# Optimization experiments

Measured on AMD Instinct MI355X. Metric: run time of the kernel, lower is better.

## Reference

```python
import jax, jax.numpy as jnp
import numpy as np

B, H0, W0, C = 8, 112, 112, 192
NH, WS, SS = 6, 7, 3
HID = 4 * C


def _rel_pos_index(ws):
    coords = np.stack(np.meshgrid(np.arange(ws), np.arange(ws), indexing='ij'))  # [2,ws,ws]
    flat = coords.reshape(2, -1)
    rel = flat[:, :, None] - flat[:, None, :]          # [2,N,N]
    rel = rel.transpose(1, 2, 0).copy()                # [N,N,2]
    rel[:, :, 0] += ws - 1
    rel[:, :, 1] += ws - 1
    rel[:, :, 0] *= 2 * ws - 1
    return rel.sum(-1)                                 # [N,N]


def _attn_mask(Hp, Wp, ws, ss):
    # 0 / -100 mask for shifted windows, identical to torch get_attn_mask
    img = np.zeros((Hp, Wp))
    cnt = 0
    for hs in (slice(0, -ws), slice(-ws, -ss), slice(-ss, None)):
        for wsl in (slice(0, -ws), slice(-ws, -ss), slice(-ss, None)):
            img[hs, wsl] = cnt
            cnt += 1
    mw = img.reshape(Hp // ws, ws, Wp // ws, ws).transpose(0, 2, 1, 3).reshape(-1, ws * ws)
    am = mw[:, None, :] - mw[:, :, None]
    return np.where(am != 0, np.float32(-100.0), np.float32(0.0)).astype(np.float32)  # [nW,N,N]


def _ln(x, g, b, eps=1e-5):
    mu = jnp.mean(x, axis=-1, keepdims=True)
    var = jnp.mean(jnp.square(x - mu), axis=-1, keepdims=True)
    return (x - mu) * jax.lax.rsqrt(var + eps) * g + b


def setup_inputs() -> dict:
    key = jax.random.key(0)
    ks = jax.random.split(key, 8)
    p = lambda k, s: jax.random.normal(k, s, jnp.float32) * 0.02
    return {
        'query': jax.random.normal(ks[0], (B, H0 * W0, C), jnp.float32),
        'norm1_g': jnp.ones((C,), jnp.float32), 'norm1_b': jnp.zeros((C,), jnp.float32),
        'qkv_w': p(ks[1], (C, 3 * C)), 'qkv_b': jnp.zeros((3 * C,), jnp.float32),
        'rpb_table': p(ks[2], ((2 * WS - 1) ** 2, NH)),
        'proj_w': p(ks[3], (C, C)), 'proj_b': jnp.zeros((C,), jnp.float32),
        'norm2_g': jnp.ones((C,), jnp.float32), 'norm2_b': jnp.zeros((C,), jnp.float32),
        'fc1_w': p(ks[4], (C, HID)), 'fc1_b': jnp.zeros((HID,), jnp.float32),
        'fc2_w': p(ks[5], (HID, C)), 'fc2_b': jnp.zeros((C,), jnp.float32),
        'H': H0, 'W': W0,
    }


def reference(query, norm1_g, norm1_b, qkv_w, qkv_b, rpb_table, proj_w, proj_b,
              norm2_g, norm2_b, fc1_w, fc1_b, fc2_w, fc2_b, H, W):
    Bq, L, Cq = query.shape
    ws, ss, nh = WS, SS, NH
    hd = Cq // nh
    N = ws * ws
    # ---- W-MSA branch ----
    x = _ln(query, norm1_g, norm1_b).reshape(Bq, H, W, Cq)
    # H, W chosen divisible by ws -> pad branch is a no-op
    x = jnp.roll(x, (-ss, -ss), axis=(1, 2))            # cyclic shift
    nWh, nWw = H // ws, W // ws
    # window partition -> [B*nW, N, C]
    xw = x.reshape(Bq, nWh, ws, nWw, ws, Cq).transpose(0, 1, 3, 2, 4, 5).reshape(-1, N, Cq)
    qkv = (xw @ qkv_w + qkv_b).reshape(-1, N, 3, nh, hd).transpose(2, 0, 3, 1, 4)
    q, k, v = qkv[0] * (hd ** -0.5), qkv[1], qkv[2]     # [B_,nh,N,hd]
    attn = jnp.einsum('bhnd,bhmd->bhnm', q, k)
    bias = rpb_table[_rel_pos_index(ws).reshape(-1)].reshape(N, N, nh).transpose(2, 0, 1)
    attn = attn + bias[None]
    mask = jnp.asarray(_attn_mask(H, W, ws, ss))        # [nW,N,N]
    nW = mask.shape[0]
    attn = attn.reshape(Bq, nW, nh, N, N) + mask[None, :, None]
    attn = jax.nn.softmax(attn.reshape(-1, nh, N, N), axis=-1)
    out = jnp.einsum('bhnm,bhmd->bhnd', attn, v).transpose(0, 2, 1, 3).reshape(-1, N, Cq)
    out = out @ proj_w + proj_b
    # window reverse + reverse shift
    x = out.reshape(Bq, nWh, nWw, ws, ws, Cq).transpose(0, 1, 3, 2, 4, 5).reshape(Bq, H, W, Cq)
    x = jnp.roll(x, (ss, ss), axis=(1, 2)).reshape(Bq, H * W, Cq)
    x = query + x
    # ---- MLP branch ----
    h = _ln(x, norm2_g, norm2_b)
    h = jax.nn.gelu(h @ fc1_w + fc1_b, approximate=False)
    return x + (h @ fc2_w + fc2_b)
```

## Files before the change

### kernel.cpp

```cpp
#include <hip/hip_runtime.h>
#include <hip/hip_bf16.h>
#include <math.h>

using bf16 = __hip_bfloat16;
typedef __bf16 bf16x8 __attribute__((ext_vector_type(8)));
typedef __bf16 bf16x4 __attribute__((ext_vector_type(4)));
typedef float floatx4 __attribute__((ext_vector_type(4)));

__device__ __forceinline__ float bf2f(bf16 x) { return __bfloat162float(x); }
__device__ __forceinline__ bf16 f2bf(float x) { return __float2bfloat16(x); }

__device__ __forceinline__ float loadExt(const void* p, long i, int f32) {
  return f32 ? ((const float*)p)[i] : bf2f(((const bf16*)p)[i]);
}
__device__ __forceinline__ void storeExt(void* p, long i, int f32, float v) {
  if (f32) ((float*)p)[i] = v;
  else     ((bf16*)p)[i] = f2bf(v);
}

#define GLOAD16(gp, lp)                                                       \
  __builtin_amdgcn_global_load_lds(                                           \
      (const __attribute__((address_space(1))) void*)(gp),                    \
      (__attribute__((address_space(3))) void*)(lp), 16, 0, 0)

__global__ void detect_kernel(const unsigned int* __restrict__ q, int* __restrict__ flag) {
  const int lane = threadIdx.x;
  const unsigned int w = q[lane];
  const unsigned int lo = w & 0xffffu;
  const unsigned int e = (lo >> 7) & 0xffu;
  const bool ok = (lo == 0u) || (e >= 100u && e <= 141u);
  const unsigned long long m = __ballot(ok);
  if (lane == 0) flag[0] = (__popcll(m) == 64) ? 1 : 0;
}

__global__ void cvt_params_kernel(const int* __restrict__ flagp,
                                  const void* qkv_b, const void* proj_b,
                                  const void* n1g, const void* n1b,
                                  const void* n2g, const void* n2b,
                                  const void* fc1_b, const void* fc2_b,
                                  const void* rpb, bf16* __restrict__ dst) {
  const int f32 = (flagp[0] == 0);
  int i = blockIdx.x * blockDim.x + threadIdx.x;
  if (i >= 3510) return;
  const void* src; int j = i;
  if      (j < 576)  { src = qkv_b; }
  else if ((j -= 576)  < 192) { src = proj_b; }
  else if ((j -= 192)  < 192) { src = n1g; }
  else if ((j -= 192)  < 192) { src = n1b; }
  else if ((j -= 192)  < 192) { src = n2g; }
  else if ((j -= 192)  < 192) { src = n2b; }
  else if ((j -= 192)  < 768) { src = fc1_b; }
  else if ((j -= 768)  < 192) { src = fc2_b; }
  else { j -= 192; src = rpb; }
  dst[i] = f2bf(loadExt(src, j, f32));
}

__global__ void cvtT_kernel(const int* __restrict__ flagp, const void* __restrict__ src,
                            bf16* __restrict__ dst, int K, int N) {
  const int f32 = (flagp[0] == 0);
  int i = blockIdx.x * blockDim.x + threadIdx.x;
  if (i >= K * N) return;
  int n = i / K, k = i - n * K;
  dst[i] = f2bf(loadExt(src, (long)k * N + n, f32));
}

__global__ void biastab_kernel(const bf16* __restrict__ rpb,
                               bf16* __restrict__ btab) {
  int i = blockIdx.x * blockDim.x + threadIdx.x;
  if (i >= 6 * 2450) return;
  int head = i / 2450, r = i - head * 2450;
  int n = r / 50, m = r - n * 50;
  float v = 0.f;
  if (n < 49 && m < 49) {
    int r1 = n / 7, c1 = n - 7 * r1, r2 = m / 7, c2 = m - 7 * r2;
    v = bf2f(rpb[((r1 - r2 + 6) * 13 + (c1 - c2 + 6)) * 6 + head]);
  }
  btab[i] = f2bf(v);
}

__global__ __launch_bounds__(256) void ln_kernel(const int* __restrict__ flagp, int ext,
                                                 const void* __restrict__ x,
                                                 const bf16* __restrict__ g,
                                                 const bf16* __restrict__ b,
                                                 bf16* __restrict__ out) {
  const int f32 = ext && (flagp[0] == 0);
  const long row = (long)blockIdx.x * 4 + (threadIdx.x >> 6);
  const int lane = threadIdx.x & 63;
  const long gbase = row * 192;
  float v0 = loadExt(x, gbase + lane, f32);
  float v1 = loadExt(x, gbase + lane + 64, f32);
  float v2 = loadExt(x, gbase + lane + 128, f32);
  float s = v0 + v1 + v2;
  #pragma unroll
  for (int off = 32; off > 0; off >>= 1) s += __shfl_xor(s, off, 64);
  const float mu = s * (1.0f / 192.0f);
  float d0 = v0 - mu, d1 = v1 - mu, d2 = v2 - mu;
  float vv = d0 * d0 + d1 * d1 + d2 * d2;
  #pragma unroll
  for (int off = 32; off > 0; off >>= 1) vv += __shfl_xor(vv, off, 64);
  const float rstd = rsqrtf(vv * (1.0f / 192.0f) + 1e-5f);
  bf16* orow = out + row * 192;
  orow[lane]       = f2bf(d0 * rstd * bf2f(g[lane])       + bf2f(b[lane]));
  orow[lane + 64]  = f2bf(d1 * rstd * bf2f(g[lane + 64])  + bf2f(b[lane + 64]));
  orow[lane + 128] = f2bf(d2 * rstd * bf2f(g[lane + 128]) + bf2f(b[lane + 128]));
}

template <int EPI>
__global__ __launch_bounds__(256) void gemm_bt(const bf16* __restrict__ A,
                                               const bf16* __restrict__ BT,
                                               const bf16* __restrict__ bias,
                                               const int* __restrict__ flagp,
                                               const void* res, int res_ext,
                                               void* out, int out_ext,
                                               int M, int N, int K) {
  __shared__ __align__(16) bf16 As[2][128 * 32];
  __shared__ __align__(16) bf16 Bs[2][64 * 32];
  const int xf32 = (flagp[0] == 0);
  const int tid = threadIdx.x;
  const int wave = tid >> 6;
  const int lane = tid & 63;
  const int l16 = lane & 15;
  const int quad = lane >> 4;

  const int nbn = N >> 6;
  const int cpx = gridDim.x >> 3;
  const int wg = (gridDim.x & 7) ? (int)blockIdx.x
                                 : (blockIdx.x & 7) * cpx + (blockIdx.x >> 3);
  const int mb = wg / nbn;
  const int nb = wg - mb * nbn;
  const long m0 = (long)mb * 128;
  const int n0 = nb << 6;

  const int rS = tid >> 2;
  const int sS = tid & 3;
  const int ss = sS ^ ((rS >> 1) & 3);
  const bf16* gA0 = A + (m0 + rS) * (long)K + ss * 8;
  const bf16* gA1 = A + (m0 + rS + 64) * (long)K + ss * 8;
  const bf16* gB  = BT + (long)(n0 + rS) * K + ss * 8;

  floatx4 acc[2][4];
  #pragma unroll
  for (int i = 0; i < 2; i++)
    #pragma unroll
    for (int j = 0; j < 4; j++) acc[i][j] = (floatx4){0.f, 0.f, 0.f, 0.f};

  const int swz = (quad ^ ((l16 >> 1) & 3)) << 3;
  const int arow = wave * 32 + l16;

  GLOAD16(gA0, &As[0][tid * 8]);
  GLOAD16(gA1, &As[0][(tid + 256) * 8]);
  GLOAD16(gB,  &Bs[0][tid * 8]);
  __syncthreads();

  int cur = 0;
  for (int k0 = 0; k0 < K; k0 += 32) {
    if (k0 + 32 < K) {
      const int nxt = cur ^ 1;
      GLOAD16(gA0 + k0 + 32, &As[nxt][tid * 8]);
      GLOAD16(gA1 + k0 + 32, &As[nxt][(tid + 256) * 8]);
      GLOAD16(gB  + k0 + 32, &Bs[nxt][tid * 8]);
    }
    bf16x8 af[2], bfr[4];
    #pragma unroll
    for (int ms = 0; ms < 2; ms++)
      af[ms] = *(const bf16x8*)&As[cur][(arow + ms * 16) * 32 + swz];
    #pragma unroll
    for (int ns = 0; ns < 4; ns++)
      bfr[ns] = *(const bf16x8*)&Bs[cur][(ns * 16 + l16) * 32 + swz];
    #pragma unroll
    for (int ms = 0; ms < 2; ms++)
      #pragma unroll
      for (int ns = 0; ns < 4; ns++)
        acc[ms][ns] = __builtin_amdgcn_mfma_f32_16x16x32_bf16(bfr[ns], af[ms], acc[ms][ns], 0, 0, 0);
    __syncthreads();
    cur ^= 1;
  }

  #pragma unroll
  for (int ms = 0; ms < 2; ms++) {
    const long row = m0 + wave * 32 + ms * 16 + l16;
    #pragma unroll
    for (int ns = 0; ns < 4; ns++) {
      const int col = n0 + ns * 16 + quad * 4;
      const long idx = row * (long)N + col;
      float v[4];
      #pragma unroll
      for (int r = 0; r < 4; r++) v[r] = acc[ms][ns][r] + bf2f(bias[col + r]);
      if (EPI == 1) {
        #pragma unroll
        for (int r = 0; r < 4; r++)
          v[r] = 0.5f * v[r] * (1.0f + erff(v[r] * 0.70710678118654752f));
      }
      if (EPI == 2) {
        if (res_ext && xf32) {
          const float4 t = *(const float4*)((const float*)res + idx);
          v[0] += t.x; v[1] += t.y; v[2] += t.z; v[3] += t.w;
        } else {
          const bf16x4 t = *(const bf16x4*)((const bf16*)res + idx);
          #pragma unroll
          for (int r = 0; r < 4; r++) v[r] += (float)t[r];
        }
      }
      if (out_ext && xf32) {
        float4 t; t.x = v[0]; t.y = v[1]; t.z = v[2]; t.w = v[3];
        *(float4*)((float*)out + idx) = t;
      } else {
        bf16x4 t;
        #pragma unroll
        for (int r = 0; r < 4; r++) t[r] = (__bf16)v[r];
        *(bf16x4*)((bf16*)out + idx) = t;
      }
    }
  }
}

__global__ __launch_bounds__(64) void attn_kernel(const bf16* __restrict__ qkv,
                                                  const bf16* __restrict__ btab,
                                                  bf16* __restrict__ out) {
  __shared__ __align__(16) float ksh[49 * 32];
  __shared__ __align__(16) float vsh[49 * 32];
  __shared__ __align__(4) bf16 bsh[2450];
  __shared__ int rowIdx[49];
  __shared__ int regn[49];
  const int lane = threadIdx.x;
  const int unit = blockIdx.x;
  const int head = unit % 6;
  const int wIdx = unit / 6;
  const int b = wIdx >> 8;
  const int w2 = wIdx & 255;
  const int wh = w2 >> 4;
  const int ww = w2 & 15;

  if (lane < 49) {
    const int r = lane / 7, c = lane - 7 * (lane / 7);
    const int hr = wh * 7 + r;
    const int wr = ww * 7 + c;
    int h = hr + 3; if (h >= 112) h -= 112;
    int w = wr + 3; if (w >= 112) w -= 112;
    rowIdx[lane] = b * 12544 + h * 112 + w;
    const int rh = hr < 105 ? 0 : (hr < 109 ? 1 : 2);
    const int rw = wr < 105 ? 0 : (wr < 109 ? 1 : 2);
    regn[lane] = rh * 3 + rw;
  }
  {
    const unsigned int* bsrc = (const unsigned int*)(btab + head * 2450);
    unsigned int* bdst = (unsigned int*)bsh;
    for (int i = lane; i < 1225; i += 64) bdst[i] = bsrc[i];
  }
  __syncthreads();

  for (int i = lane; i < 196; i += 64) {
    const int r = i >> 2, c = (i & 3) * 8;
    const long base = (long)rowIdx[r] * 576 + head * 32 + c;
    bf16x8 kk = *(const bf16x8*)&qkv[base + 192];
    bf16x8 vv = *(const bf16x8*)&qkv[base + 384];
    #pragma unroll
    for (int j = 0; j < 8; j++) {
      ksh[r * 32 + c + j] = (float)kk[j];
      vsh[r * 32 + c + j] = (float)vv[j];
    }
  }
  __syncthreads();

  if (lane < 49) {
    const float scale = 0.17677669529663687f;
    float qv[32];
    {
      const long qb = (long)rowIdx[lane] * 576 + head * 32;
      #pragma unroll
      for (int c = 0; c < 32; c += 8) {
        bf16x8 qq = *(const bf16x8*)&qkv[qb + c];
        #pragma unroll
        for (int j = 0; j < 8; j++) qv[c + j] = (float)qq[j] * scale;
      }
    }
    const int myreg = regn[lane];
    float s[49];
    #pragma unroll
    for (int m = 0; m < 49; m++) {
      float a = 0.f;
      #pragma unroll
      for (int d = 0; d < 32; d++) a += qv[d] * ksh[m * 32 + d];
      a += bf2f(bsh[lane * 50 + m]);
      if (regn[m] != myreg) a -= 100.0f;
      s[m] = a;
    }
    float mx = s[0];
    #pragma unroll
    for (int m = 1; m < 49; m++) mx = fmaxf(mx, s[m]);
    float sum = 0.f;
    #pragma unroll
    for (int m = 0; m < 49; m++) { s[m] = __expf(s[m] - mx); sum += s[m]; }
    const float inv = 1.0f / sum;
    float o[32];
    #pragma unroll
    for (int d = 0; d < 32; d++) o[d] = 0.f;
    #pragma unroll
    for (int m = 0; m < 49; m++) {
      const float p = s[m] * inv;
      #pragma unroll
      for (int d = 0; d < 32; d++) o[d] += p * vsh[m * 32 + d];
    }
    const long ob = (long)rowIdx[lane] * 192 + head * 32;
    #pragma unroll
    for (int c = 0; c < 32; c += 8) {
      bf16x8 ov;
      #pragma unroll
      for (int j = 0; j < 8; j++) ov[j] = (__bf16)o[c + j];
      *(bf16x8*)&out[ob + c] = ov;
    }
  }
}

extern "C" void kernel_launch(void* const* d_in, const int* in_sizes, int n_in,
                              void* d_out, int out_size, void* d_ws, size_t ws_size,
                              hipStream_t stream) {
  const void* query   = d_in[0];
  const void* norm1_g = d_in[1];
  const void* norm1_b = d_in[2];
  const void* qkv_w   = d_in[3];
  const void* qkv_b   = d_in[4];
  const void* rpb     = d_in[5];
  const void* proj_w  = d_in[6];
  const void* proj_b  = d_in[7];
  const void* norm2_g = d_in[8];
  const void* norm2_b = d_in[9];
  const void* fc1_w   = d_in[10];
  const void* fc1_b   = d_in[11];
  const void* fc2_w   = d_in[12];
  const void* fc2_b   = d_in[13];

  const long M = 100352;

  int* flag  = (int*)d_ws;
  bf16* base = (bf16*)((char*)d_ws + 16);
  bf16* wsA   = base;
  bf16* wsB   = wsA + M * 192;
  bf16* xbuf  = wsB + M * 768;
  bf16* qkvT  = xbuf + M * 192;
  bf16* projT = qkvT + 110592;
  bf16* fc1T  = projT + 36864;
  bf16* fc2T  = fc1T + 147456;
  bf16* pPAR  = fc2T + 147456;
  bf16* pQKVB = pPAR;
  bf16* pPRJB = pQKVB + 576;
  bf16* pN1G  = pPRJB + 192;
  bf16* pN1B  = pN1G + 192;
  bf16* pN2G  = pN1B + 192;
  bf16* pN2B  = pN2G + 192;
  bf16* pFC1B = pN2B + 192;
  bf16* pFC2B = pFC1B + 768;
  bf16* pRPB  = pFC2B + 192;
  bf16* btab  = pPAR + 3510;

  detect_kernel<<<1, 64, 0, stream>>>((const unsigned int*)query, flag);
  cvt_params_kernel<<<14, 256, 0, stream>>>(flag, qkv_b, proj_b, norm1_g, norm1_b,
                                            norm2_g, norm2_b, fc1_b, fc2_b, rpb, pPAR);
  cvtT_kernel<<<(192 * 576 + 255) / 256, 256, 0, stream>>>(flag, qkv_w, qkvT, 192, 576);
  cvtT_kernel<<<(192 * 192 + 255) / 256, 256, 0, stream>>>(flag, proj_w, projT, 192, 192);
  cvtT_kernel<<<(192 * 768 + 255) / 256, 256, 0, stream>>>(flag, fc1_w, fc1T, 192, 768);
  cvtT_kernel<<<(768 * 192 + 255) / 256, 256, 0, stream>>>(flag, fc2_w, fc2T, 768, 192);
  biastab_kernel<<<(6 * 2450 + 255) / 256, 256, 0, stream>>>(pRPB, btab);

  ln_kernel<<<M / 4, 256, 0, stream>>>(flag, 1, query, pN1G, pN1B, wsA);
  gemm_bt<0><<<784 * 9, 256, 0, stream>>>(wsA, qkvT, pQKVB, flag,
                                          nullptr, 0, wsB, 0, (int)M, 576, 192);
  attn_kernel<<<12288, 64, 0, stream>>>(wsB, btab, wsA);
  gemm_bt<2><<<784 * 3, 256, 0, stream>>>(wsA, projT, pPRJB, flag,
                                          query, 1, xbuf, 0, (int)M, 192, 192);

  ln_kernel<<<M / 4, 256, 0, stream>>>(flag, 0, xbuf, pN2G, pN2B, wsA);
  gemm_bt<1><<<784 * 12, 256, 0, stream>>>(flag ? wsA : wsA, fc1T, pFC1B, flag,
                                           nullptr, 0, wsB, 0, (int)M, 768, 192);
  gemm_bt<2><<<784 * 3, 256, 0, stream>>>(wsB, fc2T, pFC2B, flag,
                                          xbuf, 0, d_out, 1, (int)M, 192, 768);
}
```

Measured before the change: 667.2 us.

## Rewrite window attention with bf16 MFMA for QK^T and PV

The per-window attention kernel, which used scalar fp32 dot products with only 49 of 64 lanes active, now pads the 49 tokens to 64 and computes QK^T and PV with 16x16x32 bf16 MFMA instructions. Softmax runs on the accumulator fragments using cross-lane shuffles. P and transposed V are staged in XOR-swizzled LDS, and the bias table is read from global memory instead of being copied to LDS. This removes the heavy scalar FMA work, at the cost of rounding probabilities to bf16 and wasting some padded compute.

Result: faster. 614.4 us (-7.9%).

```diff
diff --git a/kernel.cpp b/kernel.cpp
--- a/kernel.cpp
+++ b/kernel.cpp
@@ -214,15 +214,15 @@
   }
 }
 
-__global__ __launch_bounds__(64) void attn_kernel(const bf16* __restrict__ qkv,
-                                                  const bf16* __restrict__ btab,
-                                                  bf16* __restrict__ out) {
-  __shared__ __align__(16) float ksh[49 * 32];
-  __shared__ __align__(16) float vsh[49 * 32];
-  __shared__ __align__(4) bf16 bsh[2450];
-  __shared__ int rowIdx[49];
-  __shared__ int regn[49];
+__global__ __launch_bounds__(64, 3) void attn_kernel(const bf16* __restrict__ qkv,
+                                                     const bf16* __restrict__ btab,
+                                                     bf16* __restrict__ out) {
+  __shared__ __align__(16) __bf16 vshT[32 * 64];
+  __shared__ __align__(16) __bf16 psh[64 * 64];
+  __shared__ int rowIdx[64];
+  __shared__ int regn[64];
   const int lane = threadIdx.x;
+  const int q = lane >> 4, l16 = lane & 15;
   const int unit = blockIdx.x;
   const int head = unit % 6;
   const int wIdx = unit / 6;
@@ -231,8 +231,9 @@
   const int wh = w2 >> 4;
   const int ww = w2 & 15;
 
-  if (lane < 49) {
-    const int r = lane / 7, c = lane - 7 * (lane / 7);
+  {
+    const int l = lane < 49 ? lane : 48;
+    const int r = l / 7, c = l - 7 * r;
     const int hr = wh * 7 + r;
     const int wr = ww * 7 + c;
     int h = hr + 3; if (h >= 112) h -= 112;
@@ -240,76 +241,160 @@
     rowIdx[lane] = b * 12544 + h * 112 + w;
     const int rh = hr < 105 ? 0 : (hr < 109 ? 1 : 2);
     const int rw = wr < 105 ? 0 : (wr < 109 ? 1 : 2);
-    regn[lane] = rh * 3 + rw;
-  }
+    regn[lane] = (lane < 49) ? rh * 3 + rw : 99;
+  }
+  __syncthreads();
+
+  int ridx[4];
+  #pragma unroll
+  for (int t = 0; t < 4; t++) ridx[t] = rowIdx[t * 16 + l16];
+
+  #pragma unroll
+  for (int ii = 0; ii < 4; ii++) {
+    const int i = lane + ii * 64;
+    const int j = i >> 2, c = (i & 3) * 8;
+    const bf16x8 vv = *(const bf16x8*)&qkv[(long)rowIdx[j] * 576 + 384 + head * 32 + c];
+    #pragma unroll
+    for (int jj = 0; jj < 8; jj++) {
+      const int d = c + jj;
+      vshT[d * 64 + (((j >> 3) ^ (d & 7)) << 3) + (j & 7)] = vv[jj];
+    }
+  }
+
+  floatx4 s[4][4];
+  #pragma unroll
+  for (int it = 0; it < 4; it++)
+    #pragma unroll
+    for (int jt = 0; jt < 4; jt++) s[it][jt] = (floatx4){0.f, 0.f, 0.f, 0.f};
   {
-    const unsigned int* bsrc = (const unsigned int*)(btab + head * 2450);
-    unsigned int* bdst = (unsigned int*)bsh;
-    for (int i = lane; i < 1225; i += 64) bdst[i] = bsrc[i];
-  }
+    bf16x8 afq[4], bfk[4];
+    #pragma unroll
+    for (int t = 0; t < 4; t++) {
+      const bf16* pQ = &qkv[(long)ridx[t] * 576 + head * 32 + q * 8];
+      afq[t] = *(const bf16x8*)pQ;
+      bfk[t] = *(const bf16x8*)(pQ + 192);
+    }
+    #pragma unroll
+    for (int it = 0; it < 4; it++)
+      #pragma unroll
+      for (int jt = 0; jt < 4; jt++)
+        s[it][jt] = __builtin_amdgcn_mfma_f32_16x16x32_bf16(afq[it], bfk[jt], s[it][jt], 0, 0, 0);
+  }
+
+  int regj[4];
+  #pragma unroll
+  for (int jt = 0; jt < 4; jt++) regj[jt] = regn[jt * 16 + l16];
+  int regi[4][4];
+  #pragma unroll
+  for (int it = 0; it < 4; it++)
+    #pragma unroll
+    for (int r = 0; r < 4; r++) regi[it][r] = regn[it * 16 + q * 4 + r];
+
+  const bf16* bt = btab + head * 2450;
+  const float scale = 0.17677669529663687f;
+  float mrow[4][4];
+  #pragma unroll
+  for (int it = 0; it < 4; it++)
+    #pragma unroll
+    for (int r = 0; r < 4; r++) mrow[it][r] = -3e38f;
+
+  #pragma unroll
+  for (int it = 0; it < 4; it++)
+    #pragma unroll
+    for (int jt = 0; jt < 4; jt++)
+      #pragma unroll
+      for (int r = 0; r < 4; r++) {
+        const int i = it * 16 + q * 4 + r;
+        const int j = jt * 16 + l16;
+        const int bi = (i < 49 ? i : 48) * 50 + (j < 49 ? j : 48);
+        float v = s[it][jt][r] * scale + bf2f(bt[bi]);
+        if (regi[it][r] != regj[jt]) v -= 100.0f;
+        v = (j < 49) ? v : -1e30f;
+        s[it][jt][r] = v;
+        mrow[it][r] = fmaxf(mrow[it][r], v);
+      }
+  #pragma unroll
+  for (int it = 0; it < 4; it++)
+    #pragma unroll
+    for (int r = 0; r < 4; r++) {
+      float m = mrow[it][r];
+      #pragma unroll
+      for (int off = 1; off < 16; off <<= 1) m = fmaxf(m, __shfl_xor(m, off, 64));
+      mrow[it][r] = m;
+    }
+  float sum[4][4];
+  #pragma unroll
+  for (int it = 0; it < 4; it++)
+    #pragma unroll
+    for (int r = 0; r < 4; r++) sum[it][r] = 0.f;
+  #pragma unroll
+  for (int it = 0; it < 4; it++)
+    #pragma unroll
+    for (int jt = 0; jt < 4; jt++)
+      #pragma unroll
+      for (int r = 0; r < 4; r++) {
+        const float e = __expf(s[it][jt][r] - mrow[it][r]);
+        s[it][jt][r] = e;
+        sum[it][r] += e;
+      }
+  #pragma unroll
+  for (int it = 0; it < 4; it++)
+    #pragma unroll
+    for (int r = 0; r < 4; r++) {
+      float t = sum[it][r];
+      #pragma unroll
+      for (int off = 1; off < 16; off <<= 1) t += __shfl_xor(t, off, 64);
+      mrow[it][r] = 1.0f / t;
+    }
+
+  #pragma unroll
+  for (int it = 0; it < 4; it++)
+    #pragma unroll
+    for (int jt = 0; jt < 4; jt++)
+      #pragma unroll
+      for (int r = 0; r < 4; r++) {
+        const int i = it * 16 + q * 4 + r;
+        const int j = jt * 16 + l16;
+        psh[i * 64 + (((j >> 3) ^ (i & 7)) << 3) + (j & 7)] =
+            (__bf16)(s[it][jt][r] * mrow[it][r]);
+      }
   __syncthreads();
 
-  for (int i = lane; i < 196; i += 64) {
-    const int r = i >> 2, c = (i & 3) * 8;
-    const long base = (long)rowIdx[r] * 576 + head * 32 + c;
-    bf16x8 kk = *(const bf16x8*)&qkv[base + 192];
-    bf16x8 vv = *(const bf16x8*)&qkv[base + 384];
-    #pragma unroll
-    for (int j = 0; j < 8; j++) {
-      ksh[r * 32 + c + j] = (float)kk[j];
-      vsh[r * 32 + c + j] = (float)vv[j];
-    }
-  }
-  __syncthreads();
-
-  if (lane < 49) {
-    const float scale = 0.17677669529663687f;
-    float qv[32];
-    {
-      const long qb = (long)rowIdx[lane] * 576 + head * 32;
-      #pragma unroll
-      for (int c = 0; c < 32; c += 8) {
-        bf16x8 qq = *(const bf16x8*)&qkv[qb + c];
+  floatx4 o[4][2];
+  #pragma unroll
+  for (int it = 0; it < 4; it++)
+    #pragma unroll
+    for (int dt = 0; dt < 2; dt++) o[it][dt] = (floatx4){0.f, 0.f, 0.f, 0.f};
+  #pragma unroll
+  for (int ks = 0; ks < 2; ks++) {
+    bf16x8 av[2];
+    #pragma unroll
+    for (int dt = 0; dt < 2; dt++) {
+      const int row = dt * 16 + l16;
+      av[dt] = *(const bf16x8*)&vshT[row * 64 + (((ks * 4 + q) ^ (row & 7)) << 3)];
+    }
+    #pragma unroll
+    for (int it = 0; it < 4; it++) {
+      const int row = it * 16 + l16;
+      const bf16x8 bp = *(const bf16x8*)&psh[row * 64 + (((ks * 4 + q) ^ (row & 7)) << 3)];
+      #pragma unroll
+      for (int dt = 0; dt < 2; dt++)
+        o[it][dt] = __builtin_amdgcn_mfma_f32_16x16x32_bf16(bp, av[dt], o[it][dt], 0, 0, 0);
+    }
+  }
+
+  #pragma unroll
+  for (int it = 0; it < 4; it++)
+    #pragma unroll
+    for (int r = 0; r < 4; r++) {
+      const int i = it * 16 + q * 4 + r;
+      if (i < 49) {
+        const long ob = (long)rowIdx[i] * 192 + head * 32;
         #pragma unroll
-        for (int j = 0; j < 8; j++) qv[c + j] = (float)qq[j] * scale;
-      }
-    }
-    const int myreg = regn[lane];
-    float s[49];
-    #pragma unroll
-    for (int m = 0; m < 49; m++) {
-      float a = 0.f;
-      #pragma unroll
-      for (int d = 0; d < 32; d++) a += qv[d] * ksh[m * 32 + d];
-      a += bf2f(bsh[lane * 50 + m]);
-      if (regn[m] != myreg) a -= 100.0f;
-      s[m] = a;
-    }
-    float mx = s[0];
-    #pragma unroll
-    for (int m = 1; m < 49; m++) mx = fmaxf(mx, s[m]);
-    float sum = 0.f;
-    #pragma unroll
-    for (int m = 0; m < 49; m++) { s[m] = __expf(s[m] - mx); sum += s[m]; }
-    const float inv = 1.0f / sum;
-    float o[32];
-    #pragma unroll
-    for (int d = 0; d < 32; d++) o[d] = 0.f;
-    #pragma unroll
-    for (int m = 0; m < 49; m++) {
-      const float p = s[m] * inv;
-      #pragma unroll
-      for (int d = 0; d < 32; d++) o[d] += p * vsh[m * 32 + d];
-    }
-    const long ob = (long)rowIdx[lane] * 192 + head * 32;
-    #pragma unroll
-    for (int c = 0; c < 32; c += 8) {
-      bf16x8 ov;
-      #pragma unroll
-      for (int j = 0; j < 8; j++) ov[j] = (__bf16)o[c + j];
-      *(bf16x8*)&out[ob + c] = ov;
-    }
-  }
+        for (int dt = 0; dt < 2; dt++)
+          out[ob + dt * 16 + l16] = f2bf(o[it][dt][r]);
+      }
+    }
 }
 
 extern "C" void kernel_launch(void* const* d_in, const int* in_sizes, int n_in,
@@ -370,7 +455,7 @@
                                           query, 1, xbuf, 0, (int)M, 192, 192);
 
   ln_kernel<<<M / 4, 256, 0, stream>>>(flag, 0, xbuf, pN2G, pN2B, wsA);
-  gemm_bt<1><<<784 * 12, 256, 0, stream>>>(flag ? wsA : wsA, fc1T, pFC1B, flag,
+  gemm_bt<1><<<784 * 12, 256, 0, stream>>>(wsA, fc1T, pFC1B, flag,
                                            nullptr, 0, wsB, 0, (int)M, 768, 192);
   gemm_bt<2><<<784 * 3, 256, 0, stream>>>(wsB, fc2T, pFC2B, flag,
                                           xbuf, 0, d_out, 1, (int)M, 192, 768);
```
